# Kernel tuning notes

Hardware: AMD Instinct MI355X
Metric: run time of the kernel (lower is better)

The kernel has to match this reference:

```python
import jax, jax.numpy as jnp
import numpy as np
from jax import lax

C = 64
K = 7
HALF = K // 2
SIGMA_MIN = 0.6
SIGMA_MAX = 1.2

_SOBEL_X = jnp.array([[-1., 0., 1.], [-2., 0., 2.], [-1., 0., 1.]], dtype=jnp.float32).reshape(1, 1, 3, 3)
_SOBEL_Y = jnp.transpose(_SOBEL_X, (0, 1, 3, 2))


def _depthwise3x3(x, kern):
    # x: [B,C,H,W]; same 3x3 kernel per channel -> fold C into batch, 1-channel conv
    B, Cc, H, W = x.shape
    y = lax.conv_general_dilated(
        x.reshape(B * Cc, 1, H, W), kern,
        window_strides=(1, 1), padding=((1, 1), (1, 1)),
        dimension_numbers=('NCHW', 'OIHW', 'NCHW'))
    return y.reshape(B, Cc, H, W)


def _shift_stack(xp, W_out, axis):
    # xp padded by HALF along `axis`; stack K shifted views along new last axis
    views = [lax.slice_in_dim(xp, i, i + W_out, axis=axis) for i in range(K)]
    return jnp.stack(views, axis=-1)


def setup_inputs() -> dict:
    key = jax.random.key(0)
    x = jax.random.normal(key, (4, C, 256, 256), dtype=jnp.float32)
    return {"x": x}


def reference(x) -> jnp.ndarray:
    B, Cc, H, W = x.shape
    # Sobel edge magnitude, mean over channels
    gx = _depthwise3x3(x, _SOBEL_X)
    gy = _depthwise3x3(x, _SOBEL_Y)
    edge = (gx ** 2 + gy ** 2).mean(axis=1, keepdims=True)  # [B,1,H,W]
    emin = edge.min(axis=(2, 3), keepdims=True)
    emax = edge.max(axis=(2, 3), keepdims=True)
    edge = (edge - emin) / (emax + 1e-6)  # note: denom = amax + eps (faithful)
    sigma = SIGMA_MIN + (SIGMA_MAX - SIGMA_MIN) * edge  # [B,1,H,W]

    # per-pixel 1D gaussian kernel, shared across channels: [B,1,H,W,K]
    offs = jnp.arange(-HALF, HALF + 1, dtype=x.dtype)
    g = jnp.exp(-(offs ** 2) / (2.0 * sigma[..., None] ** 2))
    g = g / g.sum(axis=-1, keepdims=True)

    # horizontal pass: pad W, gather K shifted views, weighted sum
    xp = jnp.pad(x, ((0, 0), (0, 0), (0, 0), (HALF, HALF)))
    out = (_shift_stack(xp, W, axis=3) * g).sum(axis=-1)
    # vertical pass with the same per-pixel kernel
    op = jnp.pad(out, ((0, 0), (0, 0), (HALF, HALF), (0, 0)))
    out = (_shift_stack(op, H, axis=2) * g).sum(axis=-1)
    return out
```

## Files before the change

kernel.cpp:

```cpp
#include <hip/hip_runtime.h>
#include <cstddef>

namespace {
constexpr int B = 4, C = 64, H = 256, W = 256;
constexpr int HW = H * W;
constexpr int CHW = C * HW;
constexpr int CG = 4;
constexpr int TH = 32;
constexpr float SMIN = 0.6f, SMAX = 1.2f;
}

__device__ __forceinline__ float4 ld4(const float* p) {
  return *(const float4*)p;
}
__device__ __forceinline__ void st4(float* p, float a, float b, float c, float d) {
  float4 v; v.x = a; v.y = b; v.z = c; v.w = d; *(float4*)p = v;
}

__global__ __launch_bounds__(256) void edge_kernel(
    const float* __restrict__ x, float* __restrict__ P,
    unsigned int* __restrict__ mm) {
  __shared__ float part[4][4][64][4];
  if (blockIdx.x == 0 && threadIdx.x < 2 * B)
    mm[threadIdx.x] = (threadIdx.x < B) ? 0x7f7fffffu : 0u;
  const int xcd = blockIdx.x & 7;
  const int slot = blockIdx.x >> 3;
  const int hbb = slot & 7;
  const int cb = slot >> 3;
  const int h0 = xcd * 32 + hbb * 4;
  const int cg = cb >> 2;
  const int b = cb & 3;
  const int lane = threadIdx.x & 63, wv = threadIdx.x >> 6;
  const float* base = x + (size_t)b * CHW + 4 * lane;
  const int c0 = cg * 16 + wv * 4;
  float acc[4][4] = {};
  #pragma unroll
  for (int cc = 0; cc < 4; ++cc) {
    const float* p = base + (size_t)(c0 + cc) * HW;
    float4 R[6];
    #pragma unroll
    for (int i = 0; i < 6; ++i) {
      const int gh = h0 - 1 + i;
      R[i] = (gh >= 0 && gh < H) ? ld4(p + (size_t)gh * W)
                                 : float4{0.f, 0.f, 0.f, 0.f};
    }
    float Lh[6], Rh[6];
    #pragma unroll
    for (int i = 0; i < 6; ++i) {
      Lh[i] = __shfl_up(R[i].w, 1);
      Rh[i] = __shfl_down(R[i].x, 1);
    }
    if (lane == 0) {
      #pragma unroll
      for (int i = 0; i < 6; ++i) Lh[i] = 0.f;
    }
    if (lane == 63) {
      #pragma unroll
      for (int i = 0; i < 6; ++i) Rh[i] = 0.f;
    }
    #pragma unroll
    for (int r = 0; r < 4; ++r) {
      const float ra[6] = {Lh[r],     R[r].x,     R[r].y,     R[r].z,     R[r].w,     Rh[r]};
      const float rb[6] = {Lh[r + 1], R[r + 1].x, R[r + 1].y, R[r + 1].z, R[r + 1].w, Rh[r + 1]};
      const float rc[6] = {Lh[r + 2], R[r + 2].x, R[r + 2].y, R[r + 2].z, R[r + 2].w, Rh[r + 2]};
      #pragma unroll
      for (int j = 0; j < 4; ++j) {
        float gx = (ra[j + 2] - ra[j]) + 2.f * (rb[j + 2] - rb[j]) + (rc[j + 2] - rc[j]);
        float gy = (rc[j] - ra[j]) + 2.f * (rc[j + 1] - ra[j + 1]) + (rc[j + 2] - ra[j + 2]);
        acc[r][j] = fmaf(gx, gx, acc[r][j]);
        acc[r][j] = fmaf(gy, gy, acc[r][j]);
      }
    }
  }
  #pragma unroll
  for (int r = 0; r < 4; ++r)
    #pragma unroll
    for (int j = 0; j < 4; ++j) part[wv][r][lane][j] = acc[r][j];
  __syncthreads();
  {
    const int r = wv;
    float s[4];
    #pragma unroll
    for (int j = 0; j < 4; ++j)
      s[j] = part[0][r][lane][j] + part[1][r][lane][j] +
             part[2][r][lane][j] + part[3][r][lane][j];
    st4(P + (size_t)(cg * B + b) * HW + (size_t)(h0 + r) * W + 4 * lane,
        s[0], s[1], s[2], s[3]);
  }
}

__global__ __launch_bounds__(256) void combine_kernel(
    const float* __restrict__ P, float* __restrict__ edge,
    unsigned int* __restrict__ mm) {
  __shared__ float smn[4], smx[4];
  const int t = blockIdx.x * 256 + threadIdx.x;
  const int pix4 = t * 4;
  const int b = pix4 >> 16;
  const int off = pix4 & (HW - 1);
  float4 s0 = ld4(P + (size_t)(0 * B + b) * HW + off);
  float4 s1 = ld4(P + (size_t)(1 * B + b) * HW + off);
  float4 s2 = ld4(P + (size_t)(2 * B + b) * HW + off);
  float4 s3 = ld4(P + (size_t)(3 * B + b) * HW + off);
  float e0 = (s0.x + s1.x + s2.x + s3.x) * (1.f / 64.f);
  float e1 = (s0.y + s1.y + s2.y + s3.y) * (1.f / 64.f);
  float e2 = (s0.z + s1.z + s2.z + s3.z) * (1.f / 64.f);
  float e3 = (s0.w + s1.w + s2.w + s3.w) * (1.f / 64.f);
  st4(edge + pix4, e0, e1, e2, e3);
  float mn = fminf(fminf(e0, e1), fminf(e2, e3));
  float mx = fmaxf(fmaxf(e0, e1), fmaxf(e2, e3));
  #pragma unroll
  for (int o = 32; o > 0; o >>= 1) {
    mn = fminf(mn, __shfl_down(mn, o, 64));
    mx = fmaxf(mx, __shfl_down(mx, o, 64));
  }
  const int lane = threadIdx.x & 63, wv = threadIdx.x >> 6;
  if (lane == 0) { smn[wv] = mn; smx[wv] = mx; }
  __syncthreads();
  if (threadIdx.x == 0) {
    mn = fminf(fminf(smn[0], smn[1]), fminf(smn[2], smn[3]));
    mx = fmaxf(fmaxf(smx[0], smx[1]), fmaxf(smx[2], smx[3]));
    atomicMin(mm + b, __float_as_uint(mn));
    atomicMax(mm + B + b, __float_as_uint(mx));
  }
}

__global__ __launch_bounds__(256) void weights_kernel(
    const float* __restrict__ edge, const unsigned int* __restrict__ mm,
    float* __restrict__ wt) {
  const int t = blockIdx.x * 256 + threadIdx.x;
  const int pix4 = t * 4;
  const int b = pix4 >> 16;
  const float emin = __uint_as_float(mm[b]);
  const float inv_den = 1.f / (__uint_as_float(mm[B + b]) + 1e-6f);
  float4 ev = ld4(edge + pix4);
  const float E[4] = {ev.x, ev.y, ev.z, ev.w};
  float r[8];
  #pragma unroll
  for (int j = 0; j < 4; ++j) {
    float en = (E[j] - emin) * inv_den;
    float sg = SMIN + (SMAX - SMIN) * en;
    float a = 1.0f / (2.0f * sg * sg);
    float e1 = __expf(-a);
    float t2 = e1 * e1, e4 = t2 * t2, e9 = e4 * e4 * e1;
    float inv = 1.f / (1.f + 2.f * (e1 + e4 + e9));
    r[2 * j] = e1; r[2 * j + 1] = inv;
  }
  st4(wt + (size_t)pix4 * 2,     r[0], r[1], r[2], r[3]);
  st4(wt + (size_t)pix4 * 2 + 4, r[4], r[5], r[6], r[7]);
}

__device__ __forceinline__ void recon_g(float e1, float inv, float g[7]) {
  float t2 = e1 * e1, e4 = t2 * t2, e9 = e4 * e4 * e1;
  g[3] = inv; g[2] = e1 * inv; g[1] = e4 * inv; g[0] = e9 * inv;
  g[4] = g[2]; g[5] = g[1]; g[6] = g[0];
}

__global__ __launch_bounds__(256) void fusedblur_kernel(
    const float* __restrict__ x, const float* __restrict__ wt,
    float* __restrict__ out) {
  __shared__ float hb[TH + 6][W];
  const int xcd = blockIdx.x & 7;
  const int slot = blockIdx.x >> 3;
  const int s = slot & 7;
  const int bc = xcd * 32 + (slot >> 3);
  const int b = bc >> 6;
  const int h0 = s * TH;
  const int lane = threadIdx.x & 63, wv = threadIdx.x >> 6;
  const float* xp = x + (size_t)bc * HW + 4 * lane;
  const float* wp = wt + (size_t)b * HW * 2 + 8 * lane;
  float* op = out + (size_t)bc * HW + 4 * lane;

  for (int r = wv; r < TH + 6; r += 4) {
    const int gh = h0 - 3 + r;
    float4 o = {0.f, 0.f, 0.f, 0.f};
    if (gh >= 0 && gh < H) {
      float4 v = ld4(xp + (size_t)gh * W);
      float4 q0 = ld4(wp + (size_t)gh * W * 2);
      float4 q1 = ld4(wp + (size_t)gh * W * 2 + 4);
      float L1 = __shfl_up(v.y, 1), L2 = __shfl_up(v.z, 1), L3 = __shfl_up(v.w, 1);
      float R1 = __shfl_down(v.x, 1), R2 = __shfl_down(v.y, 1), R3 = __shfl_down(v.z, 1);
      if (lane == 0)  { L1 = 0.f; L2 = 0.f; L3 = 0.f; }
      if (lane == 63) { R1 = 0.f; R2 = 0.f; R3 = 0.f; }
      const float win[10] = {L1, L2, L3, v.x, v.y, v.z, v.w, R1, R2, R3};
      const float E1[4] = {q0.x, q0.z, q1.x, q1.z};
      const float IV[4] = {q0.y, q0.w, q1.y, q1.w};
      float acc[4];
      #pragma unroll
      for (int j = 0; j < 4; ++j) {
        float g[7]; recon_g(E1[j], IV[j], g);
        float sacc = g[0] * win[j];
        #pragma unroll
        for (int i = 1; i < 7; ++i) sacc = fmaf(g[i], win[j + i], sacc);
        acc[j] = sacc;
      }
      o.x = acc[0]; o.y = acc[1]; o.z = acc[2]; o.w = acc[3];
    }
    *(float4*)&hb[r][4 * lane] = o;
  }
  __syncthreads();

  const int r0 = wv * 8;
  float win7[7][4];
  #pragma unroll
  for (int i = 0; i < 7; ++i) {
    float4 v = *(const float4*)&hb[r0 + i][4 * lane];
    win7[i][0] = v.x; win7[i][1] = v.y; win7[i][2] = v.z; win7[i][3] = v.w;
  }
  #pragma unroll
  for (int k = 0; k < 8; ++k) {
    const int gh = h0 + r0 + k;
    float4 q0 = ld4(wp + (size_t)gh * W * 2);
    float4 q1 = ld4(wp + (size_t)gh * W * 2 + 4);
    const float E1[4] = {q0.x, q0.z, q1.x, q1.z};
    const float IV[4] = {q0.y, q0.w, q1.y, q1.w};
    float acc[4];
    #pragma unroll
    for (int j = 0; j < 4; ++j) {
      float g[7]; recon_g(E1[j], IV[j], g);
      float sacc = g[0] * win7[0][j];
      #pragma unroll
      for (int i = 1; i < 7; ++i) sacc = fmaf(g[i], win7[i][j], sacc);
      acc[j] = sacc;
    }
    st4(op + (size_t)gh * W, acc[0], acc[1], acc[2], acc[3]);
    if (k < 7) {
      #pragma unroll
      for (int i = 0; i < 6; ++i) {
        #pragma unroll
        for (int j = 0; j < 4; ++j) win7[i][j] = win7[i + 1][j];
      }
      float4 nv = *(const float4*)&hb[r0 + k + 7][4 * lane];
      win7[6][0] = nv.x; win7[6][1] = nv.y; win7[6][2] = nv.z; win7[6][3] = nv.w;
    }
  }
}

extern "C" void kernel_launch(void* const* d_in, const int* in_sizes, int n_in,
                              void* d_out, int out_size, void* d_ws, size_t ws_size,
                              hipStream_t stream) {
  const float* x = (const float*)d_in[0];
  float* out = (float*)d_out;

  unsigned int* mm = (unsigned int*)d_ws;
  float* edge = (float*)((char*)d_ws + 1024);
  float* wt = (float*)((char*)d_ws + 1024 + (size_t)B * HW * 4);

  float* P = out;

  edge_kernel<<<B * CG * (H / 4), 256, 0, stream>>>(x, P, mm);
  combine_kernel<<<(B * HW / 4) / 256, 256, 0, stream>>>(P, edge, mm);
  weights_kernel<<<(B * HW / 4) / 256, 256, 0, stream>>>(edge, mm, wt);
  fusedblur_kernel<<<B * C * (H / TH), 256, 0, stream>>>(x, wt, out);
}
```

Before: 141.7 us.

## Fuse edge combine, min/max and weight computation into edge and blur kernels

Pipeline goes from four kernels to two. The edge kernel now reduces all 64 channels per block, so it writes the final edge map directly plus per-band min/max partials instead of using atomics. The blur kernel reduces those 64 partials with wave shuffles and recomputes the Gaussian weights per pixel from the edge value, which drops the separate weights buffer. The blur is also folded to use symmetric pairs. This removes launches and intermediate traffic, but edge_kernel now launches only 256 blocks with a 16-channel serial loop each, and the exp and divide work is redone in both blur passes for every channel.

```diff
diff --git a/kernel.cpp b/kernel.cpp
--- a/kernel.cpp
+++ b/kernel.cpp
@@ -5,7 +5,6 @@
 constexpr int B = 4, C = 64, H = 256, W = 256;
 constexpr int HW = H * W;
 constexpr int CHW = C * HW;
-constexpr int CG = 4;
 constexpr int TH = 32;
 constexpr float SMIN = 0.6f, SMAX = 1.2f;
 }
@@ -18,25 +17,21 @@
 }
 
 __global__ __launch_bounds__(256) void edge_kernel(
-    const float* __restrict__ x, float* __restrict__ P,
-    unsigned int* __restrict__ mm) {
+    const float* __restrict__ x, float* __restrict__ edge,
+    float* __restrict__ mmp) {
   __shared__ float part[4][4][64][4];
-  if (blockIdx.x == 0 && threadIdx.x < 2 * B)
-    mm[threadIdx.x] = (threadIdx.x < B) ? 0x7f7fffffu : 0u;
+  __shared__ float rmn[4], rmx[4];
   const int xcd = blockIdx.x & 7;
   const int slot = blockIdx.x >> 3;
   const int hbb = slot & 7;
-  const int cb = slot >> 3;
+  const int b = slot >> 3;
   const int h0 = xcd * 32 + hbb * 4;
-  const int cg = cb >> 2;
-  const int b = cb & 3;
   const int lane = threadIdx.x & 63, wv = threadIdx.x >> 6;
-  const float* base = x + (size_t)b * CHW + 4 * lane;
-  const int c0 = cg * 16 + wv * 4;
+  const float* base = x + (size_t)b * CHW + (size_t)(wv * 16) * HW + 4 * lane;
   float acc[4][4] = {};
-  #pragma unroll
-  for (int cc = 0; cc < 4; ++cc) {
-    const float* p = base + (size_t)(c0 + cc) * HW;
+  #pragma unroll 4
+  for (int cc = 0; cc < 16; ++cc) {
+    const float* p = base + (size_t)cc * HW;
     float4 R[6];
     #pragma unroll
     for (int i = 0; i < 6; ++i) {
@@ -77,87 +72,54 @@
     #pragma unroll
     for (int j = 0; j < 4; ++j) part[wv][r][lane][j] = acc[r][j];
   __syncthreads();
-  {
-    const int r = wv;
-    float s[4];
-    #pragma unroll
-    for (int j = 0; j < 4; ++j)
-      s[j] = part[0][r][lane][j] + part[1][r][lane][j] +
-             part[2][r][lane][j] + part[3][r][lane][j];
-    st4(P + (size_t)(cg * B + b) * HW + (size_t)(h0 + r) * W + 4 * lane,
-        s[0], s[1], s[2], s[3]);
-  }
-}
-
-__global__ __launch_bounds__(256) void combine_kernel(
-    const float* __restrict__ P, float* __restrict__ edge,
-    unsigned int* __restrict__ mm) {
-  __shared__ float smn[4], smx[4];
-  const int t = blockIdx.x * 256 + threadIdx.x;
-  const int pix4 = t * 4;
-  const int b = pix4 >> 16;
-  const int off = pix4 & (HW - 1);
-  float4 s0 = ld4(P + (size_t)(0 * B + b) * HW + off);
-  float4 s1 = ld4(P + (size_t)(1 * B + b) * HW + off);
-  float4 s2 = ld4(P + (size_t)(2 * B + b) * HW + off);
-  float4 s3 = ld4(P + (size_t)(3 * B + b) * HW + off);
-  float e0 = (s0.x + s1.x + s2.x + s3.x) * (1.f / 64.f);
-  float e1 = (s0.y + s1.y + s2.y + s3.y) * (1.f / 64.f);
-  float e2 = (s0.z + s1.z + s2.z + s3.z) * (1.f / 64.f);
-  float e3 = (s0.w + s1.w + s2.w + s3.w) * (1.f / 64.f);
-  st4(edge + pix4, e0, e1, e2, e3);
-  float mn = fminf(fminf(e0, e1), fminf(e2, e3));
-  float mx = fmaxf(fmaxf(e0, e1), fmaxf(e2, e3));
+  const int r = wv;
+  float s[4];
+  #pragma unroll
+  for (int j = 0; j < 4; ++j)
+    s[j] = (part[0][r][lane][j] + part[1][r][lane][j] +
+            part[2][r][lane][j] + part[3][r][lane][j]) * (1.f / 64.f);
+  st4(edge + (size_t)b * HW + (size_t)(h0 + r) * W + 4 * lane,
+      s[0], s[1], s[2], s[3]);
+  float mn = fminf(fminf(s[0], s[1]), fminf(s[2], s[3]));
+  float mx = fmaxf(fmaxf(s[0], s[1]), fmaxf(s[2], s[3]));
   #pragma unroll
   for (int o = 32; o > 0; o >>= 1) {
     mn = fminf(mn, __shfl_down(mn, o, 64));
     mx = fmaxf(mx, __shfl_down(mx, o, 64));
   }
-  const int lane = threadIdx.x & 63, wv = threadIdx.x >> 6;
-  if (lane == 0) { smn[wv] = mn; smx[wv] = mx; }
+  if (lane == 0) { rmn[wv] = mn; rmx[wv] = mx; }
   __syncthreads();
   if (threadIdx.x == 0) {
-    mn = fminf(fminf(smn[0], smn[1]), fminf(smn[2], smn[3]));
-    mx = fmaxf(fmaxf(smx[0], smx[1]), fmaxf(smx[2], smx[3]));
-    atomicMin(mm + b, __float_as_uint(mn));
-    atomicMax(mm + B + b, __float_as_uint(mx));
-  }
-}
-
-__global__ __launch_bounds__(256) void weights_kernel(
-    const float* __restrict__ edge, const unsigned int* __restrict__ mm,
-    float* __restrict__ wt) {
-  const int t = blockIdx.x * 256 + threadIdx.x;
-  const int pix4 = t * 4;
-  const int b = pix4 >> 16;
-  const float emin = __uint_as_float(mm[b]);
-  const float inv_den = 1.f / (__uint_as_float(mm[B + b]) + 1e-6f);
-  float4 ev = ld4(edge + pix4);
-  const float E[4] = {ev.x, ev.y, ev.z, ev.w};
-  float r[8];
-  #pragma unroll
-  for (int j = 0; j < 4; ++j) {
-    float en = (E[j] - emin) * inv_den;
-    float sg = SMIN + (SMAX - SMIN) * en;
-    float a = 1.0f / (2.0f * sg * sg);
-    float e1 = __expf(-a);
-    float t2 = e1 * e1, e4 = t2 * t2, e9 = e4 * e4 * e1;
-    float inv = 1.f / (1.f + 2.f * (e1 + e4 + e9));
-    r[2 * j] = e1; r[2 * j + 1] = inv;
-  }
-  st4(wt + (size_t)pix4 * 2,     r[0], r[1], r[2], r[3]);
-  st4(wt + (size_t)pix4 * 2 + 4, r[4], r[5], r[6], r[7]);
-}
-
-__device__ __forceinline__ void recon_g(float e1, float inv, float g[7]) {
+    mn = fminf(fminf(rmn[0], rmn[1]), fminf(rmn[2], rmn[3]));
+    mx = fmaxf(fmaxf(rmx[0], rmx[1]), fmaxf(rmx[2], rmx[3]));
+    const int band = xcd * 8 + hbb;
+    mmp[2 * (b * 64 + band)] = mn;
+    mmp[2 * (b * 64 + band) + 1] = mx;
+  }
+}
+
+__device__ __forceinline__ void wt_px(float e, float emin, float inv_den,
+                                      float& e1, float& iv) {
+  float en = (e - emin) * inv_den;
+  float sg = SMIN + (SMAX - SMIN) * en;
+  float a = __fdividef(1.0f, 2.0f * sg * sg);
+  e1 = __expf(-a);
   float t2 = e1 * e1, e4 = t2 * t2, e9 = e4 * e4 * e1;
-  g[3] = inv; g[2] = e1 * inv; g[1] = e4 * inv; g[0] = e9 * inv;
-  g[4] = g[2]; g[5] = g[1]; g[6] = g[0];
+  iv = __fdividef(1.0f, 1.f + 2.f * (e1 + e4 + e9));
+}
+
+__device__ __forceinline__ float blur7(const float* w, float e1, float iv) {
+  float t2 = e1 * e1, e4 = t2 * t2, e9 = e4 * e4 * e1;
+  float u = w[3];
+  u = fmaf(e1, w[2] + w[4], u);
+  u = fmaf(e4, w[1] + w[5], u);
+  u = fmaf(e9, w[0] + w[6], u);
+  return u * iv;
 }
 
 __global__ __launch_bounds__(256) void fusedblur_kernel(
-    const float* __restrict__ x, const float* __restrict__ wt,
-    float* __restrict__ out) {
+    const float* __restrict__ x, const float* __restrict__ edge,
+    const float* __restrict__ mmp, float* __restrict__ out) {
   __shared__ float hb[TH + 6][W];
   const int xcd = blockIdx.x & 7;
   const int slot = blockIdx.x >> 3;
@@ -166,8 +128,19 @@
   const int b = bc >> 6;
   const int h0 = s * TH;
   const int lane = threadIdx.x & 63, wv = threadIdx.x >> 6;
+
+  float2 mv = *(const float2*)&mmp[2 * (b * 64 + lane)];
+  float mn = mv.x, mx = mv.y;
+  #pragma unroll
+  for (int o = 1; o < 64; o <<= 1) {
+    mn = fminf(mn, __shfl_xor(mn, o, 64));
+    mx = fmaxf(mx, __shfl_xor(mx, o, 64));
+  }
+  const float emin = mn;
+  const float inv_den = 1.f / (mx + 1e-6f);
+
   const float* xp = x + (size_t)bc * HW + 4 * lane;
-  const float* wp = wt + (size_t)b * HW * 2 + 8 * lane;
+  const float* ep = edge + (size_t)b * HW + 4 * lane;
   float* op = out + (size_t)bc * HW + 4 * lane;
 
   for (int r = wv; r < TH + 6; r += 4) {
@@ -175,23 +148,19 @@
     float4 o = {0.f, 0.f, 0.f, 0.f};
     if (gh >= 0 && gh < H) {
       float4 v = ld4(xp + (size_t)gh * W);
-      float4 q0 = ld4(wp + (size_t)gh * W * 2);
-      float4 q1 = ld4(wp + (size_t)gh * W * 2 + 4);
+      float4 ev = ld4(ep + (size_t)gh * W);
       float L1 = __shfl_up(v.y, 1), L2 = __shfl_up(v.z, 1), L3 = __shfl_up(v.w, 1);
       float R1 = __shfl_down(v.x, 1), R2 = __shfl_down(v.y, 1), R3 = __shfl_down(v.z, 1);
       if (lane == 0)  { L1 = 0.f; L2 = 0.f; L3 = 0.f; }
       if (lane == 63) { R1 = 0.f; R2 = 0.f; R3 = 0.f; }
       const float win[10] = {L1, L2, L3, v.x, v.y, v.z, v.w, R1, R2, R3};
-      const float E1[4] = {q0.x, q0.z, q1.x, q1.z};
-      const float IV[4] = {q0.y, q0.w, q1.y, q1.w};
+      const float E[4] = {ev.x, ev.y, ev.z, ev.w};
       float acc[4];
       #pragma unroll
       for (int j = 0; j < 4; ++j) {
-        float g[7]; recon_g(E1[j], IV[j], g);
-        float sacc = g[0] * win[j];
-        #pragma unroll
-        for (int i = 1; i < 7; ++i) sacc = fmaf(g[i], win[j + i], sacc);
-        acc[j] = sacc;
+        float e1, iv;
+        wt_px(E[j], emin, inv_den, e1, iv);
+        acc[j] = blur7(win + j, e1, iv);
       }
       o.x = acc[0]; o.y = acc[1]; o.z = acc[2]; o.w = acc[3];
     }
@@ -209,18 +178,17 @@
   #pragma unroll
   for (int k = 0; k < 8; ++k) {
     const int gh = h0 + r0 + k;
-    float4 q0 = ld4(wp + (size_t)gh * W * 2);
-    float4 q1 = ld4(wp + (size_t)gh * W * 2 + 4);
-    const float E1[4] = {q0.x, q0.z, q1.x, q1.z};
-    const float IV[4] = {q0.y, q0.w, q1.y, q1.w};
+    float4 ev = ld4(ep + (size_t)gh * W);
+    const float E[4] = {ev.x, ev.y, ev.z, ev.w};
     float acc[4];
     #pragma unroll
     for (int j = 0; j < 4; ++j) {
-      float g[7]; recon_g(E1[j], IV[j], g);
-      float sacc = g[0] * win7[0][j];
-      #pragma unroll
-      for (int i = 1; i < 7; ++i) sacc = fmaf(g[i], win7[i][j], sacc);
-      acc[j] = sacc;
+      float e1, iv;
+      wt_px(E[j], emin, inv_den, e1, iv);
+      float col[7];
+      #pragma unroll
+      for (int i = 0; i < 7; ++i) col[i] = win7[i][j];
+      acc[j] = blur7(col, e1, iv);
     }
     st4(op + (size_t)gh * W, acc[0], acc[1], acc[2], acc[3]);
     if (k < 7) {
@@ -241,14 +209,9 @@
   const float* x = (const float*)d_in[0];
   float* out = (float*)d_out;
 
-  unsigned int* mm = (unsigned int*)d_ws;
-  float* edge = (float*)((char*)d_ws + 1024);
-  float* wt = (float*)((char*)d_ws + 1024 + (size_t)B * HW * 4);
-
-  float* P = out;
-
-  edge_kernel<<<B * CG * (H / 4), 256, 0, stream>>>(x, P, mm);
-  combine_kernel<<<(B * HW / 4) / 256, 256, 0, stream>>>(P, edge, mm);
-  weights_kernel<<<(B * HW / 4) / 256, 256, 0, stream>>>(edge, mm, wt);
-  fusedblur_kernel<<<B * C * (H / TH), 256, 0, stream>>>(x, wt, out);
-}
+  float* edge = (float*)d_ws;
+  float* mmp = (float*)((char*)d_ws + (size_t)B * HW * 4);
+
+  edge_kernel<<<B * (H / 4), 256, 0, stream>>>(x, edge, mmp);
+  fusedblur_kernel<<<B * C * (H / TH), 256, 0, stream>>>(x, edge, mmp, out);
+}
```

Measured after the change: 156.2 us. 10.3% more time.

## Fuse channel-group combine into edge kernel with 1024-thread blocks, drop atomics

Applied to the files above, without the earlier changes.

The edge kernel now covers all 64 channels in one 1024-thread block, reducing the per-wave partials in shared memory and writing the final mean edge map directly. This removes the combine kernel, its partial-sum buffer traffic and one launch. Global min/max atomics are replaced by per-band partial results that the weights kernel reduces with wave shuffles, which also removes the workspace init. The cost is fewer, larger blocks (256 blocks of 1024 threads), a 64 KB shared buffer that may limit occupancy, and a 16-way reduction in shared memory.

```diff
diff --git a/kernel.cpp b/kernel.cpp
--- a/kernel.cpp
+++ b/kernel.cpp
@@ -5,7 +5,6 @@
 constexpr int B = 4, C = 64, H = 256, W = 256;
 constexpr int HW = H * W;
 constexpr int CHW = C * HW;
-constexpr int CG = 4;
 constexpr int TH = 32;
 constexpr float SMIN = 0.6f, SMAX = 1.2f;
 }
@@ -17,26 +16,22 @@
   float4 v; v.x = a; v.y = b; v.z = c; v.w = d; *(float4*)p = v;
 }
 
-__global__ __launch_bounds__(256) void edge_kernel(
-    const float* __restrict__ x, float* __restrict__ P,
-    unsigned int* __restrict__ mm) {
-  __shared__ float part[4][4][64][4];
-  if (blockIdx.x == 0 && threadIdx.x < 2 * B)
-    mm[threadIdx.x] = (threadIdx.x < B) ? 0x7f7fffffu : 0u;
+__global__ __launch_bounds__(1024) void edge_kernel(
+    const float* __restrict__ x, float* __restrict__ edge,
+    float* __restrict__ mmp) {
+  __shared__ float part[16][4][64][4];
+  __shared__ float rmn[4], rmx[4];
   const int xcd = blockIdx.x & 7;
   const int slot = blockIdx.x >> 3;
   const int hbb = slot & 7;
-  const int cb = slot >> 3;
+  const int b = slot >> 3;
   const int h0 = xcd * 32 + hbb * 4;
-  const int cg = cb >> 2;
-  const int b = cb & 3;
   const int lane = threadIdx.x & 63, wv = threadIdx.x >> 6;
-  const float* base = x + (size_t)b * CHW + 4 * lane;
-  const int c0 = cg * 16 + wv * 4;
+  const float* base = x + (size_t)b * CHW + (size_t)(wv * 4) * HW + 4 * lane;
   float acc[4][4] = {};
   #pragma unroll
   for (int cc = 0; cc < 4; ++cc) {
-    const float* p = base + (size_t)(c0 + cc) * HW;
+    const float* p = base + (size_t)cc * HW;
     float4 R[6];
     #pragma unroll
     for (int i = 0; i < 6; ++i) {
@@ -77,61 +72,53 @@
     #pragma unroll
     for (int j = 0; j < 4; ++j) part[wv][r][lane][j] = acc[r][j];
   __syncthreads();
-  {
+  if (wv < 4) {
     const int r = wv;
-    float s[4];
-    #pragma unroll
-    for (int j = 0; j < 4; ++j)
-      s[j] = part[0][r][lane][j] + part[1][r][lane][j] +
-             part[2][r][lane][j] + part[3][r][lane][j];
-    st4(P + (size_t)(cg * B + b) * HW + (size_t)(h0 + r) * W + 4 * lane,
+    float s[4] = {};
+    #pragma unroll
+    for (int w = 0; w < 16; ++w) {
+      #pragma unroll
+      for (int j = 0; j < 4; ++j) s[j] += part[w][r][lane][j];
+    }
+    #pragma unroll
+    for (int j = 0; j < 4; ++j) s[j] *= (1.f / 64.f);
+    st4(edge + (size_t)b * HW + (size_t)(h0 + r) * W + 4 * lane,
         s[0], s[1], s[2], s[3]);
-  }
-}
-
-__global__ __launch_bounds__(256) void combine_kernel(
-    const float* __restrict__ P, float* __restrict__ edge,
-    unsigned int* __restrict__ mm) {
-  __shared__ float smn[4], smx[4];
-  const int t = blockIdx.x * 256 + threadIdx.x;
-  const int pix4 = t * 4;
-  const int b = pix4 >> 16;
-  const int off = pix4 & (HW - 1);
-  float4 s0 = ld4(P + (size_t)(0 * B + b) * HW + off);
-  float4 s1 = ld4(P + (size_t)(1 * B + b) * HW + off);
-  float4 s2 = ld4(P + (size_t)(2 * B + b) * HW + off);
-  float4 s3 = ld4(P + (size_t)(3 * B + b) * HW + off);
-  float e0 = (s0.x + s1.x + s2.x + s3.x) * (1.f / 64.f);
-  float e1 = (s0.y + s1.y + s2.y + s3.y) * (1.f / 64.f);
-  float e2 = (s0.z + s1.z + s2.z + s3.z) * (1.f / 64.f);
-  float e3 = (s0.w + s1.w + s2.w + s3.w) * (1.f / 64.f);
-  st4(edge + pix4, e0, e1, e2, e3);
-  float mn = fminf(fminf(e0, e1), fminf(e2, e3));
-  float mx = fmaxf(fmaxf(e0, e1), fmaxf(e2, e3));
-  #pragma unroll
-  for (int o = 32; o > 0; o >>= 1) {
-    mn = fminf(mn, __shfl_down(mn, o, 64));
-    mx = fmaxf(mx, __shfl_down(mx, o, 64));
-  }
-  const int lane = threadIdx.x & 63, wv = threadIdx.x >> 6;
-  if (lane == 0) { smn[wv] = mn; smx[wv] = mx; }
+    float mn = fminf(fminf(s[0], s[1]), fminf(s[2], s[3]));
+    float mx = fmaxf(fmaxf(s[0], s[1]), fmaxf(s[2], s[3]));
+    #pragma unroll
+    for (int o = 32; o > 0; o >>= 1) {
+      mn = fminf(mn, __shfl_down(mn, o, 64));
+      mx = fmaxf(mx, __shfl_down(mx, o, 64));
+    }
+    if (lane == 0) { rmn[r] = mn; rmx[r] = mx; }
+  }
   __syncthreads();
   if (threadIdx.x == 0) {
-    mn = fminf(fminf(smn[0], smn[1]), fminf(smn[2], smn[3]));
-    mx = fmaxf(fmaxf(smx[0], smx[1]), fmaxf(smx[2], smx[3]));
-    atomicMin(mm + b, __float_as_uint(mn));
-    atomicMax(mm + B + b, __float_as_uint(mx));
+    float mn = fminf(fminf(rmn[0], rmn[1]), fminf(rmn[2], rmn[3]));
+    float mx = fmaxf(fmaxf(rmx[0], rmx[1]), fmaxf(rmx[2], rmx[3]));
+    const int band = xcd * 8 + hbb;
+    mmp[2 * (b * 64 + band)] = mn;
+    mmp[2 * (b * 64 + band) + 1] = mx;
   }
 }
 
 __global__ __launch_bounds__(256) void weights_kernel(
-    const float* __restrict__ edge, const unsigned int* __restrict__ mm,
+    const float* __restrict__ edge, const float* __restrict__ mmp,
     float* __restrict__ wt) {
   const int t = blockIdx.x * 256 + threadIdx.x;
   const int pix4 = t * 4;
   const int b = pix4 >> 16;
-  const float emin = __uint_as_float(mm[b]);
-  const float inv_den = 1.f / (__uint_as_float(mm[B + b]) + 1e-6f);
+  const int lane = threadIdx.x & 63;
+  float2 mv = *(const float2*)&mmp[2 * (b * 64 + lane)];
+  float mn = mv.x, mx = mv.y;
+  #pragma unroll
+  for (int o = 1; o < 64; o <<= 1) {
+    mn = fminf(mn, __shfl_xor(mn, o, 64));
+    mx = fmaxf(mx, __shfl_xor(mx, o, 64));
+  }
+  const float emin = mn;
+  const float inv_den = 1.f / (mx + 1e-6f);
   float4 ev = ld4(edge + pix4);
   const float E[4] = {ev.x, ev.y, ev.z, ev.w};
   float r[8];
@@ -241,14 +228,11 @@
   const float* x = (const float*)d_in[0];
   float* out = (float*)d_out;
 
-  unsigned int* mm = (unsigned int*)d_ws;
-  float* edge = (float*)((char*)d_ws + 1024);
-  float* wt = (float*)((char*)d_ws + 1024 + (size_t)B * HW * 4);
-
-  float* P = out;
-
-  edge_kernel<<<B * CG * (H / 4), 256, 0, stream>>>(x, P, mm);
-  combine_kernel<<<(B * HW / 4) / 256, 256, 0, stream>>>(P, edge, mm);
-  weights_kernel<<<(B * HW / 4) / 256, 256, 0, stream>>>(edge, mm, wt);
+  float* mmp = (float*)d_ws;
+  float* edge = (float*)((char*)d_ws + 4096);
+  float* wt = (float*)((char*)d_ws + 4096 + (size_t)B * HW * 4);
+
+  edge_kernel<<<B * (H / 4), 1024, 0, stream>>>(x, edge, mmp);
+  weights_kernel<<<(B * HW / 4) / 256, 256, 0, stream>>>(edge, mmp, wt);
   fusedblur_kernel<<<B * C * (H / TH), 256, 0, stream>>>(x, wt, out);
 }
```

New measurement: 183.4 us. 29.4% more time.

## Replace global atomic min/max with per-block partials and halve blur row tile

Applied to the files above, without the earlier changes.

The combine kernel now writes per-block min/max partials to a workspace array instead of doing global atomics, and the weights kernel reduces the 64 partials per batch with a wave-wide xor shuffle. This removes the mm initialisation in the edge kernel and atomic contention. The blur tile height drops from 32 to 16 rows, doubling the block count for more parallelism at the cost of more halo recomputation (22 vs 38 rows per 16 vs 32 outputs). The partial buffer P moves from the output buffer to the workspace.

```diff
diff --git a/kernel.cpp b/kernel.cpp
--- a/kernel.cpp
+++ b/kernel.cpp
@@ -6,7 +6,7 @@
 constexpr int HW = H * W;
 constexpr int CHW = C * HW;
 constexpr int CG = 4;
-constexpr int TH = 32;
+constexpr int TH = 16;
 constexpr float SMIN = 0.6f, SMAX = 1.2f;
 }
 
@@ -18,11 +18,8 @@
 }
 
 __global__ __launch_bounds__(256) void edge_kernel(
-    const float* __restrict__ x, float* __restrict__ P,
-    unsigned int* __restrict__ mm) {
+    const float* __restrict__ x, float* __restrict__ P) {
   __shared__ float part[4][4][64][4];
-  if (blockIdx.x == 0 && threadIdx.x < 2 * B)
-    mm[threadIdx.x] = (threadIdx.x < B) ? 0x7f7fffffu : 0u;
   const int xcd = blockIdx.x & 7;
   const int slot = blockIdx.x >> 3;
   const int hbb = slot & 7;
@@ -91,7 +88,7 @@
 
 __global__ __launch_bounds__(256) void combine_kernel(
     const float* __restrict__ P, float* __restrict__ edge,
-    unsigned int* __restrict__ mm) {
+    float* __restrict__ mmp) {
   __shared__ float smn[4], smx[4];
   const int t = blockIdx.x * 256 + threadIdx.x;
   const int pix4 = t * 4;
@@ -119,19 +116,27 @@
   if (threadIdx.x == 0) {
     mn = fminf(fminf(smn[0], smn[1]), fminf(smn[2], smn[3]));
     mx = fmaxf(fmaxf(smx[0], smx[1]), fmaxf(smx[2], smx[3]));
-    atomicMin(mm + b, __float_as_uint(mn));
-    atomicMax(mm + B + b, __float_as_uint(mx));
+    mmp[2 * (b * 64 + (blockIdx.x & 63))] = mn;
+    mmp[2 * (b * 64 + (blockIdx.x & 63)) + 1] = mx;
   }
 }
 
 __global__ __launch_bounds__(256) void weights_kernel(
-    const float* __restrict__ edge, const unsigned int* __restrict__ mm,
+    const float* __restrict__ edge, const float* __restrict__ mmp,
     float* __restrict__ wt) {
   const int t = blockIdx.x * 256 + threadIdx.x;
   const int pix4 = t * 4;
   const int b = pix4 >> 16;
-  const float emin = __uint_as_float(mm[b]);
-  const float inv_den = 1.f / (__uint_as_float(mm[B + b]) + 1e-6f);
+  const int lane = threadIdx.x & 63;
+  float2 mv = *(const float2*)&mmp[2 * (b * 64 + lane)];
+  float mn = mv.x, mx = mv.y;
+  #pragma unroll
+  for (int o = 1; o < 64; o <<= 1) {
+    mn = fminf(mn, __shfl_xor(mn, o, 64));
+    mx = fmaxf(mx, __shfl_xor(mx, o, 64));
+  }
+  const float emin = mn;
+  const float inv_den = 1.f / (mx + 1e-6f);
   float4 ev = ld4(edge + pix4);
   const float E[4] = {ev.x, ev.y, ev.z, ev.w};
   float r[8];
@@ -161,8 +166,8 @@
   __shared__ float hb[TH + 6][W];
   const int xcd = blockIdx.x & 7;
   const int slot = blockIdx.x >> 3;
-  const int s = slot & 7;
-  const int bc = xcd * 32 + (slot >> 3);
+  const int s = slot & 15;
+  const int bc = xcd * 32 + (slot >> 4);
   const int b = bc >> 6;
   const int h0 = s * TH;
   const int lane = threadIdx.x & 63, wv = threadIdx.x >> 6;
@@ -199,7 +204,7 @@
   }
   __syncthreads();
 
-  const int r0 = wv * 8;
+  const int r0 = wv * 4;
   float win7[7][4];
   #pragma unroll
   for (int i = 0; i < 7; ++i) {
@@ -207,7 +212,7 @@
     win7[i][0] = v.x; win7[i][1] = v.y; win7[i][2] = v.z; win7[i][3] = v.w;
   }
   #pragma unroll
-  for (int k = 0; k < 8; ++k) {
+  for (int k = 0; k < 4; ++k) {
     const int gh = h0 + r0 + k;
     float4 q0 = ld4(wp + (size_t)gh * W * 2);
     float4 q1 = ld4(wp + (size_t)gh * W * 2 + 4);
@@ -223,7 +228,7 @@
       acc[j] = sacc;
     }
     st4(op + (size_t)gh * W, acc[0], acc[1], acc[2], acc[3]);
-    if (k < 7) {
+    if (k < 3) {
       #pragma unroll
       for (int i = 0; i < 6; ++i) {
         #pragma unroll
@@ -241,14 +246,13 @@
   const float* x = (const float*)d_in[0];
   float* out = (float*)d_out;
 
-  unsigned int* mm = (unsigned int*)d_ws;
-  float* edge = (float*)((char*)d_ws + 1024);
-  float* wt = (float*)((char*)d_ws + 1024 + (size_t)B * HW * 4);
-
-  float* P = out;
-
-  edge_kernel<<<B * CG * (H / 4), 256, 0, stream>>>(x, P, mm);
-  combine_kernel<<<(B * HW / 4) / 256, 256, 0, stream>>>(P, edge, mm);
-  weights_kernel<<<(B * HW / 4) / 256, 256, 0, stream>>>(edge, mm, wt);
+  float* mmp = (float*)d_ws;
+  float* edge = (float*)((char*)d_ws + 4096);
+  float* wt = (float*)((char*)d_ws + 4096 + (size_t)B * HW * 4);
+  float* P = (float*)((char*)d_ws + 4096 + (size_t)B * HW * 12);
+
+  edge_kernel<<<B * CG * (H / 4), 256, 0, stream>>>(x, P);
+  combine_kernel<<<(B * HW / 4) / 256, 256, 0, stream>>>(P, edge, mmp);
+  weights_kernel<<<(B * HW / 4) / 256, 256, 0, stream>>>(edge, mmp, wt);
   fusedblur_kernel<<<B * C * (H / TH), 256, 0, stream>>>(x, wt, out);
 }
```

Result: no change. 139.5 us (-1.6%).
